# Performance work log

Hardware: AMD Instinct MI355X
Metric: run time of the kernel (lower is better)

## Reference

```python
import jax, jax.numpy as jnp
import numpy as np

B, H, W, D = 4, 64, 64, 256
NH = 8
HD = D // NH        # 32
R = 2               # reduction_ratio
SCALE = 1.0 / np.sqrt(HD).astype(np.float32)
EPS = 1e-5


def _layernorm(x, g, b):
    m = jnp.mean(x, axis=-1, keepdims=True)
    v = jnp.mean((x - m) ** 2, axis=-1, keepdims=True)
    return (x - m) * jax.lax.rsqrt(v + EPS) * g + b


def setup_inputs() -> dict:
    key = jax.random.key(0)
    ks = jax.random.split(key, 8)
    s = 0.02
    return {
        "x": jax.random.normal(ks[0], (B, H, W, D), jnp.float32),
        "de": jax.random.normal(ks[1], (B, H, W, D), jnp.float32),  # unused by module
        "ln1_g": jnp.ones((D,), jnp.float32),
        "ln1_b": jnp.zeros((D,), jnp.float32),
        "Wq": jax.random.normal(ks[2], (D, D), jnp.float32) * s,
        "bq": jnp.zeros((D,), jnp.float32),
        "Wk": jax.random.normal(ks[3], (D, D), jnp.float32) * s,
        "bk": jnp.zeros((D,), jnp.float32),
        "Wv": jax.random.normal(ks[4], (D, D), jnp.float32) * s,
        "bv": jnp.zeros((D,), jnp.float32),
        "Wmean": jax.random.normal(ks[5], (D, D), jnp.float32) * s,  # no bias
        "ln2_g": jnp.ones((D,), jnp.float32),
        "ln2_b": jnp.zeros((D,), jnp.float32),
        "Wo": jax.random.normal(ks[6], (D, D), jnp.float32) * s,
        "bo": jnp.zeros((D,), jnp.float32),
    }


def reference(x, de, ln1_g, ln1_b, Wq, bq, Wk, bk, Wv, bv, Wmean, ln2_g, ln2_b, Wo, bo):
    b, h, w, d = x.shape
    identity = x
    x_norm = _layernorm(x, ln1_g, ln1_b)
    q = x_norm @ Wq + bq                                   # [b,h,w,d]
    # shift_size == 0 -> no roll. Block-mean pool K/V by factor R.
    x_red = jnp.mean(x.reshape(b, h // R, R, w // R, R, d), axis=(2, 4))  # [b,h/R,w/R,d]
    x_red = x_red @ Wmean
    x_red_norm = _layernorm(x_red, ln2_g, ln2_b)
    k = x_red_norm @ Wk + bk
    v = x_red_norm @ Wv + bv
    # split heads: [b, NH, N, HD]
    qf = q.reshape(b, h * w, NH, HD).transpose(0, 2, 1, 3)
    kf = k.reshape(b, (h // R) * (w // R), NH, HD).transpose(0, 2, 1, 3)
    vf = v.reshape(b, (h // R) * (w // R), NH, HD).transpose(0, 2, 1, 3)
    attn = jax.nn.softmax(jnp.einsum('bhqd,bhkd->bhqk', qf, kf) * SCALE, axis=-1)
    out = jnp.einsum('bhqk,bhkd->bhqd', attn, vf)          # [b,NH,N,HD]
    out = out.transpose(0, 2, 1, 3).reshape(b, h, w, d)
    out = out @ Wo + bo
    out = out + identity
    return out, attn
```

## Files before the change

kernel.cpp:

```cpp
#include <hip/hip_runtime.h>

typedef __bf16 bf16x8 __attribute__((ext_vector_type(8)));
typedef __bf16 bf16x4 __attribute__((ext_vector_type(4)));
typedef float f32x4 __attribute__((ext_vector_type(4)));

#define SCALE 0.17677669529663687f

__global__ __launch_bounds__(256) void castw_kernel(const float* __restrict__ W,
    __bf16* __restrict__ Wt) {
  int id = blockIdx.x * 256 + threadIdx.x;
  int kk = id >> 8, n = id & 255;
  Wt[n * 256 + kk] = (__bf16)W[id];
}

__global__ __launch_bounds__(256) void ln_fp32_kernel(const float* __restrict__ in,
    const float* __restrict__ g, const float* __restrict__ bb,
    __bf16* __restrict__ out) {
  int wid = (blockIdx.x * 256 + threadIdx.x) >> 6;
  int lane = threadIdx.x & 63;
  const float4 v = *(const float4*)(in + (size_t)wid * 256 + lane * 4);
  float s = v.x + v.y + v.z + v.w;
  #pragma unroll
  for (int off = 32; off; off >>= 1) s += __shfl_down(s, off);
  float mean = __shfl(s, 0) * (1.0f / 256.0f);
  float dx = v.x - mean, dy = v.y - mean, dz = v.z - mean, dw = v.w - mean;
  float vs = dx * dx + dy * dy + dz * dz + dw * dw;
  #pragma unroll
  for (int off = 32; off; off >>= 1) vs += __shfl_down(vs, off);
  float rstd = rsqrtf(__shfl(vs, 0) * (1.0f / 256.0f) + 1e-5f);
  const float4 gg = *(const float4*)(g + lane * 4);
  const float4 bv = *(const float4*)(bb + lane * 4);
  bf16x4 o4;
  o4[0] = (__bf16)(dx * rstd * gg.x + bv.x);
  o4[1] = (__bf16)(dy * rstd * gg.y + bv.y);
  o4[2] = (__bf16)(dz * rstd * gg.z + bv.z);
  o4[3] = (__bf16)(dw * rstd * gg.w + bv.w);
  *(bf16x4*)(out + (size_t)wid * 256 + lane * 4) = o4;
}

__global__ __launch_bounds__(256) void ln_bf16_kernel(const __bf16* __restrict__ in,
    const float* __restrict__ g, const float* __restrict__ bb,
    __bf16* __restrict__ out) {
  int wid = (blockIdx.x * 256 + threadIdx.x) >> 6;
  int lane = threadIdx.x & 63;
  bf16x4 iv = *(const bf16x4*)(in + (size_t)wid * 256 + lane * 4);
  float vx = (float)iv[0], vy = (float)iv[1], vz = (float)iv[2], vw = (float)iv[3];
  float s = vx + vy + vz + vw;
  #pragma unroll
  for (int off = 32; off; off >>= 1) s += __shfl_down(s, off);
  float mean = __shfl(s, 0) * (1.0f / 256.0f);
  float dx = vx - mean, dy = vy - mean, dz = vz - mean, dw = vw - mean;
  float vs = dx * dx + dy * dy + dz * dz + dw * dw;
  #pragma unroll
  for (int off = 32; off; off >>= 1) vs += __shfl_down(vs, off);
  float rstd = rsqrtf(__shfl(vs, 0) * (1.0f / 256.0f) + 1e-5f);
  const float4 gg = *(const float4*)(g + lane * 4);
  const float4 bv = *(const float4*)(bb + lane * 4);
  bf16x4 o4;
  o4[0] = (__bf16)(dx * rstd * gg.x + bv.x);
  o4[1] = (__bf16)(dy * rstd * gg.y + bv.y);
  o4[2] = (__bf16)(dz * rstd * gg.z + bv.z);
  o4[3] = (__bf16)(dw * rstd * gg.w + bv.w);
  *(bf16x4*)(out + (size_t)wid * 256 + lane * 4) = o4;
}

__global__ __launch_bounds__(256) void pool_kernel(const float* __restrict__ x,
    __bf16* __restrict__ xp) {
  int idx = blockIdx.x * 256 + threadIdx.x;
  int t = idx >> 6, c4 = (idx & 63) << 2;
  int b = t >> 10, rem = t & 1023;
  int i = rem >> 5, j = rem & 31;
  size_t base = ((size_t)b * 4096 + i * 128 + j * 2) * 256 + c4;
  float4 a0 = *(const float4*)(x + base);
  float4 a1 = *(const float4*)(x + base + 256);
  float4 a2 = *(const float4*)(x + base + 16384);
  float4 a3 = *(const float4*)(x + base + 16640);
  bf16x4 o4;
  o4[0] = (__bf16)(0.25f * (a0.x + a1.x + a2.x + a3.x));
  o4[1] = (__bf16)(0.25f * (a0.y + a1.y + a2.y + a3.y));
  o4[2] = (__bf16)(0.25f * (a0.z + a1.z + a2.z + a3.z));
  o4[3] = (__bf16)(0.25f * (a0.w + a1.w + a2.w + a3.w));
  *(bf16x4*)(xp + (size_t)t * 256 + c4) = o4;
}

__global__ __launch_bounds__(256) void gemm_mfma(
    const __bf16* __restrict__ A, const __bf16* __restrict__ Wt,
    const float* __restrict__ bias, const float* __restrict__ resid,
    void* __restrict__ Cout, int mode) {
  const int tid = threadIdx.x;
  const int w = tid >> 6, l = tid & 63;
  const int col = l & 15, quad = l >> 4;
  const int row0 = blockIdx.x * 64 + w * 16;
  const int col0 = blockIdx.y * 64;
  f32x4 acc[4] = {{0.f,0.f,0.f,0.f},{0.f,0.f,0.f,0.f},{0.f,0.f,0.f,0.f},{0.f,0.f,0.f,0.f}};
  const __bf16* ap = A + (size_t)(row0 + col) * 256 + quad * 8;
  #pragma unroll
  for (int ks = 0; ks < 8; ++ks) {
    bf16x8 af = *(const bf16x8*)(ap + ks * 32);
    #pragma unroll
    for (int n = 0; n < 4; ++n) {
      bf16x8 bf = *(const bf16x8*)(Wt + (size_t)(col0 + n * 16 + col) * 256 + ks * 32 + quad * 8);
      acc[n] = __builtin_amdgcn_mfma_f32_16x16x32_bf16(af, bf, acc[n], 0, 0, 0);
    }
  }
  const int rbase = row0 + quad * 4;
  #pragma unroll
  for (int n = 0; n < 4; ++n) {
    const int cc = col0 + n * 16 + col;
    const float bv = bias ? bias[cc] : 0.0f;
    if (mode == 0) {
      __bf16* C = (__bf16*)Cout;
      #pragma unroll
      for (int r = 0; r < 4; ++r)
        C[(size_t)(rbase + r) * 256 + cc] = (__bf16)(acc[n][r] + bv);
    } else if (mode == 1) {
      __bf16* C = (__bf16*)Cout;
      const int bb2 = rbase >> 10, tl = rbase & 1023;
      bf16x4 o4;
      #pragma unroll
      for (int r = 0; r < 4; ++r) o4[r] = (__bf16)(acc[n][r] + bv);
      *(bf16x4*)(C + ((size_t)(bb2 * 256 + cc)) * 1024 + tl) = o4;
    } else {
      float* C = (float*)Cout;
      #pragma unroll
      for (int r = 0; r < 4; ++r) {
        size_t off = (size_t)(rbase + r) * 256 + cc;
        C[off] = acc[n][r] + bv + resid[off];
      }
    }
  }
}

__device__ __forceinline__ int swz(int row, int c) {
  return row * 1024 + (c ^ ((row & 3) << 3));
}

__global__ __launch_bounds__(256) void attn_fused(
    const __bf16* __restrict__ q, const __bf16* __restrict__ kb,
    const __bf16* __restrict__ vT, float* __restrict__ attn,
    __bf16* __restrict__ oat) {
  __shared__ float Ss[16 * 1024];
  const int tid = threadIdx.x;
  const int w = tid >> 6, l = tid & 63;
  const int col = l & 15, quad = l >> 4;
  const int bh = blockIdx.y, b = bh >> 3, h = bh & 7;
  const int q0 = blockIdx.x * 16;

  bf16x8 qf = *(const bf16x8*)(q + ((size_t)(b * 4096 + q0 + col)) * 256 + h * 32 + quad * 8);
  const __bf16* kbase = kb + ((size_t)(b * 1024 + col)) * 256 + h * 32 + quad * 8;
  #pragma unroll 4
  for (int t = 0; t < 16; ++t) {
    int j0 = w * 256 + t * 16;
    bf16x8 kf = *(const bf16x8*)(kbase + (size_t)j0 * 256);
    f32x4 c = {0.f, 0.f, 0.f, 0.f};
    c = __builtin_amdgcn_mfma_f32_16x16x32_bf16(qf, kf, c, 0, 0, 0);
    #pragma unroll
    for (int r = 0; r < 4; ++r)
      Ss[swz(quad * 4 + r, j0 + col)] = c[r] * SCALE;
  }
  __syncthreads();

  #pragma unroll
  for (int rr = 0; rr < 4; ++rr) {
    int row = w * 4 + rr;
    float4 v4[4];
    float m = -1e30f;
    #pragma unroll
    for (int i = 0; i < 4; ++i) {
      v4[i] = *(const float4*)(&Ss[swz(row, i * 256 + l * 4)]);
      m = fmaxf(m, fmaxf(fmaxf(v4[i].x, v4[i].y), fmaxf(v4[i].z, v4[i].w)));
    }
    #pragma unroll
    for (int off = 32; off; off >>= 1) m = fmaxf(m, __shfl_down(m, off));
    m = __shfl(m, 0);
    float s = 0.f;
    #pragma unroll
    for (int i = 0; i < 4; ++i) {
      v4[i].x = __expf(v4[i].x - m); v4[i].y = __expf(v4[i].y - m);
      v4[i].z = __expf(v4[i].z - m); v4[i].w = __expf(v4[i].w - m);
      s += v4[i].x + v4[i].y + v4[i].z + v4[i].w;
    }
    #pragma unroll
    for (int off = 32; off; off >>= 1) s += __shfl_down(s, off);
    float inv = 1.0f / __shfl(s, 0);
    float* arow = attn + ((size_t)bh * 4096 + q0 + row) * 1024;
    #pragma unroll
    for (int i = 0; i < 4; ++i) {
      v4[i].x *= inv; v4[i].y *= inv; v4[i].z *= inv; v4[i].w *= inv;
      *(float4*)(arow + i * 256 + l * 4) = v4[i];
      *(float4*)(&Ss[swz(row, i * 256 + l * 4)]) = v4[i];
    }
  }
  __syncthreads();

  f32x4 a0 = {0.f, 0.f, 0.f, 0.f}, a1 = {0.f, 0.f, 0.f, 0.f};
  const __bf16* v0p = vT + ((size_t)(b * 256 + h * 32 + col)) * 1024;
  const __bf16* v1p = v0p + 16 * 1024;
  #pragma unroll 2
  for (int s8 = 0; s8 < 8; ++s8) {
    int k0 = w * 256 + s8 * 32;
    int base = swz(col, k0 + quad * 8);
    f32x4 p0 = *(const f32x4*)(&Ss[base]);
    f32x4 p1 = *(const f32x4*)(&Ss[base + 4]);
    bf16x8 af;
    af[0] = (__bf16)p0[0]; af[1] = (__bf16)p0[1]; af[2] = (__bf16)p0[2]; af[3] = (__bf16)p0[3];
    af[4] = (__bf16)p1[0]; af[5] = (__bf16)p1[1]; af[6] = (__bf16)p1[2]; af[7] = (__bf16)p1[3];
    bf16x8 b0 = *(const bf16x8*)(v0p + k0 + quad * 8);
    bf16x8 b1 = *(const bf16x8*)(v1p + k0 + quad * 8);
    a0 = __builtin_amdgcn_mfma_f32_16x16x32_bf16(af, b0, a0, 0, 0, 0);
    a1 = __builtin_amdgcn_mfma_f32_16x16x32_bf16(af, b1, a1, 0, 0, 0);
  }
  __syncthreads();

  float* part = Ss;
  #pragma unroll
  for (int r = 0; r < 4; ++r) {
    part[(w * 16 + quad * 4 + r) * 32 + col] = a0[r];
    part[(w * 16 + quad * 4 + r) * 32 + 16 + col] = a1[r];
  }
  __syncthreads();
  int idx = tid;
  #pragma unroll
  for (int it = 0; it < 2; ++it, idx += 256) {
    int row = idx >> 5, d = idx & 31;
    float sum = part[row * 32 + d] + part[(16 + row) * 32 + d]
              + part[(32 + row) * 32 + d] + part[(48 + row) * 32 + d];
    oat[((size_t)(b * 4096 + q0 + row)) * 256 + h * 32 + d] = (__bf16)sum;
  }
}

extern "C" void kernel_launch(void* const* d_in, const int* in_sizes, int n_in,
                              void* d_out, int out_size, void* d_ws, size_t ws_size,
                              hipStream_t stream) {
  (void)in_sizes; (void)n_in; (void)out_size; (void)ws_size;
  const float* x     = (const float*)d_in[0];
  const float* ln1_g = (const float*)d_in[2];
  const float* ln1_b = (const float*)d_in[3];
  const float* Wq    = (const float*)d_in[4];
  const float* bq    = (const float*)d_in[5];
  const float* Wk    = (const float*)d_in[6];
  const float* bk    = (const float*)d_in[7];
  const float* Wv    = (const float*)d_in[8];
  const float* bv    = (const float*)d_in[9];
  const float* Wmean = (const float*)d_in[10];
  const float* ln2_g = (const float*)d_in[11];
  const float* ln2_b = (const float*)d_in[12];
  const float* Wo    = (const float*)d_in[13];
  const float* bo    = (const float*)d_in[14];

  float* out  = (float*)d_out;
  float* attn = out + 4194304;

  __bf16* w0   = (__bf16*)d_ws;
  __bf16* xn   = w0;
  __bf16* qb   = w0 + 4194304;
  __bf16* oat  = w0 + 8388608;
  __bf16* xp   = w0 + 12582912;
  __bf16* xrm  = w0 + 13631488;
  __bf16* xr   = w0 + 14680064;
  __bf16* kbuf = w0 + 15728640;
  __bf16* vTb  = w0 + 16777216;
  __bf16* WtQ  = w0 + 17825792;
  __bf16* WtK  = WtQ + 65536;
  __bf16* WtV  = WtK + 65536;
  __bf16* WtM  = WtV + 65536;
  __bf16* WtO  = WtM + 65536;

  castw_kernel<<<256, 256, 0, stream>>>(Wq, WtQ);
  castw_kernel<<<256, 256, 0, stream>>>(Wk, WtK);
  castw_kernel<<<256, 256, 0, stream>>>(Wv, WtV);
  castw_kernel<<<256, 256, 0, stream>>>(Wmean, WtM);
  castw_kernel<<<256, 256, 0, stream>>>(Wo, WtO);

  ln_fp32_kernel<<<4096, 256, 0, stream>>>(x, ln1_g, ln1_b, xn);
  gemm_mfma<<<dim3(256, 4), 256, 0, stream>>>(xn, WtQ, bq, nullptr, qb, 0);
  pool_kernel<<<1024, 256, 0, stream>>>(x, xp);
  gemm_mfma<<<dim3(64, 4), 256, 0, stream>>>(xp, WtM, nullptr, nullptr, xrm, 0);
  ln_bf16_kernel<<<1024, 256, 0, stream>>>(xrm, ln2_g, ln2_b, xr);
  gemm_mfma<<<dim3(64, 4), 256, 0, stream>>>(xr, WtK, bk, nullptr, kbuf, 0);
  gemm_mfma<<<dim3(64, 4), 256, 0, stream>>>(xr, WtV, bv, nullptr, vTb, 1);
  attn_fused<<<dim3(256, 32), 256, 0, stream>>>(qb, kbuf, vTb, attn, oat);
  gemm_mfma<<<dim3(256, 4), 256, 0, stream>>>(oat, WtO, bo, x, (void*)out, 2);
}
```

Baseline: 783.1 us.

## Defer softmax normalization and write attn probs coalesced with nontemporal stores

Merges the five weight-cast launches into one grid that selects its weight by block index. In the attention kernel, softmax normalization is deferred: unnormalized exponentials are kept in LDS and the PV result is scaled by a per-row inverse sum. The fp32 attention probabilities are written at the end with a whole-block coalesced nontemporal store loop. It also changes the LDS swizzle pattern and uses a separate partial-sum buffer so one barrier can be dropped, at the cost of extra shared memory.

Measured after the change: 741.0 us. 1.06x faster.

```diff
diff --git a/kernel.cpp b/kernel.cpp
--- a/kernel.cpp
+++ b/kernel.cpp
@@ -6,11 +6,19 @@
 
 #define SCALE 0.17677669529663687f
 
-__global__ __launch_bounds__(256) void castw_kernel(const float* __restrict__ W,
-    __bf16* __restrict__ Wt) {
-  int id = blockIdx.x * 256 + threadIdx.x;
+__global__ __launch_bounds__(256) void castw_kernel(
+    const float* __restrict__ W0, const float* __restrict__ W1,
+    const float* __restrict__ W2, const float* __restrict__ W3,
+    const float* __restrict__ W4,
+    __bf16* __restrict__ T0, __bf16* __restrict__ T1,
+    __bf16* __restrict__ T2, __bf16* __restrict__ T3,
+    __bf16* __restrict__ T4) {
+  int which = blockIdx.x >> 8;
+  const float* W = which == 0 ? W0 : which == 1 ? W1 : which == 2 ? W2 : which == 3 ? W3 : W4;
+  __bf16* T = which == 0 ? T0 : which == 1 ? T1 : which == 2 ? T2 : which == 3 ? T3 : T4;
+  int id = (blockIdx.x & 255) * 256 + threadIdx.x;
   int kk = id >> 8, n = id & 255;
-  Wt[n * 256 + kk] = (__bf16)W[id];
+  T[n * 256 + kk] = (__bf16)W[id];
 }
 
 __global__ __launch_bounds__(256) void ln_fp32_kernel(const float* __restrict__ in,
@@ -132,7 +140,7 @@
 }
 
 __device__ __forceinline__ int swz(int row, int c) {
-  return row * 1024 + (c ^ ((row & 3) << 3));
+  return row * 1024 + (c ^ ((row & 7) << 2));
 }
 
 __global__ __launch_bounds__(256) void attn_fused(
@@ -140,6 +148,8 @@
     const __bf16* __restrict__ vT, float* __restrict__ attn,
     __bf16* __restrict__ oat) {
   __shared__ float Ss[16 * 1024];
+  __shared__ float part[64 * 32];
+  __shared__ float inv_s[16];
   const int tid = threadIdx.x;
   const int w = tid >> 6, l = tid & 63;
   const int col = l & 15, quad = l >> 4;
@@ -182,14 +192,10 @@
     }
     #pragma unroll
     for (int off = 32; off; off >>= 1) s += __shfl_down(s, off);
-    float inv = 1.0f / __shfl(s, 0);
-    float* arow = attn + ((size_t)bh * 4096 + q0 + row) * 1024;
-    #pragma unroll
-    for (int i = 0; i < 4; ++i) {
-      v4[i].x *= inv; v4[i].y *= inv; v4[i].z *= inv; v4[i].w *= inv;
-      *(float4*)(arow + i * 256 + l * 4) = v4[i];
+    if (l == 0) inv_s[row] = 1.0f / __shfl(s, 0);
+    #pragma unroll
+    for (int i = 0; i < 4; ++i)
       *(float4*)(&Ss[swz(row, i * 256 + l * 4)]) = v4[i];
-    }
   }
   __syncthreads();
 
@@ -199,9 +205,9 @@
   #pragma unroll 2
   for (int s8 = 0; s8 < 8; ++s8) {
     int k0 = w * 256 + s8 * 32;
-    int base = swz(col, k0 + quad * 8);
-    f32x4 p0 = *(const f32x4*)(&Ss[base]);
-    f32x4 p1 = *(const f32x4*)(&Ss[base + 4]);
+    int c0 = k0 + quad * 8;
+    f32x4 p0 = *(const f32x4*)(&Ss[swz(col, c0)]);
+    f32x4 p1 = *(const f32x4*)(&Ss[swz(col, c0 + 4)]);
     bf16x8 af;
     af[0] = (__bf16)p0[0]; af[1] = (__bf16)p0[1]; af[2] = (__bf16)p0[2]; af[3] = (__bf16)p0[3];
     af[4] = (__bf16)p1[0]; af[5] = (__bf16)p1[1]; af[6] = (__bf16)p1[2]; af[7] = (__bf16)p1[3];
@@ -210,9 +216,7 @@
     a0 = __builtin_amdgcn_mfma_f32_16x16x32_bf16(af, b0, a0, 0, 0, 0);
     a1 = __builtin_amdgcn_mfma_f32_16x16x32_bf16(af, b1, a1, 0, 0, 0);
   }
-  __syncthreads();
-
-  float* part = Ss;
+
   #pragma unroll
   for (int r = 0; r < 4; ++r) {
     part[(w * 16 + quad * 4 + r) * 32 + col] = a0[r];
@@ -223,9 +227,19 @@
   #pragma unroll
   for (int it = 0; it < 2; ++it, idx += 256) {
     int row = idx >> 5, d = idx & 31;
-    float sum = part[row * 32 + d] + part[(16 + row) * 32 + d]
-              + part[(32 + row) * 32 + d] + part[(48 + row) * 32 + d];
+    float sum = (part[row * 32 + d] + part[(16 + row) * 32 + d]
+               + part[(32 + row) * 32 + d] + part[(48 + row) * 32 + d]) * inv_s[row];
     oat[((size_t)(b * 4096 + q0 + row)) * 256 + h * 32 + d] = (__bf16)sum;
+  }
+
+  float* abase = attn + ((size_t)bh * 4096 + q0) * 1024;
+  int c4 = tid * 4;
+  #pragma unroll 4
+  for (int row = 0; row < 16; ++row) {
+    f32x4 pv = *(const f32x4*)(&Ss[swz(row, c4)]);
+    float iv = inv_s[row];
+    pv[0] *= iv; pv[1] *= iv; pv[2] *= iv; pv[3] *= iv;
+    __builtin_nontemporal_store(pv, (f32x4*)(abase + (size_t)row * 1024 + c4));
   }
 }
 
@@ -266,11 +280,7 @@
   __bf16* WtM  = WtV + 65536;
   __bf16* WtO  = WtM + 65536;
 
-  castw_kernel<<<256, 256, 0, stream>>>(Wq, WtQ);
-  castw_kernel<<<256, 256, 0, stream>>>(Wk, WtK);
-  castw_kernel<<<256, 256, 0, stream>>>(Wv, WtV);
-  castw_kernel<<<256, 256, 0, stream>>>(Wmean, WtM);
-  castw_kernel<<<256, 256, 0, stream>>>(Wo, WtO);
+  castw_kernel<<<1280, 256, 0, stream>>>(Wq, Wk, Wv, Wmean, Wo, WtQ, WtK, WtV, WtM, WtO);
 
   ln_fp32_kernel<<<4096, 256, 0, stream>>>(x, ln1_g, ln1_b, xn);
   gemm_mfma<<<dim3(256, 4), 256, 0, stream>>>(xn, WtQ, bq, nullptr, qb, 0);
```
